# Performance work log

Hardware: AMD Instinct MI355X
Metric: run time of the kernel (lower is better)

The kernel has to match this reference:

```python
import jax, jax.numpy as jnp
import numpy as np

N_NODES = 100000


def setup_inputs() -> dict:
    key = jax.random.key(0)
    k1, k2, k3, k4, k5 = jax.random.split(key, 5)
    K, N, Z, F = 2, N_NODES, 128, 128
    E = 1600000
    x = jax.random.normal(k1, (K, N, Z), dtype=jnp.float32)
    adj_rows = jax.random.randint(k2, (E,), 0, N, dtype=jnp.int32)
    adj_cols = jax.random.randint(k3, (E,), 0, N, dtype=jnp.int32)
    adj_vals = jax.random.uniform(k4, (E,), dtype=jnp.float32)
    # xavier_uniform_ for [Z, F]
    limit = float(np.sqrt(6.0 / (Z + F)))
    weight = jax.random.uniform(k5, (Z, F), dtype=jnp.float32, minval=-limit, maxval=limit)
    return {"x": x, "adj_rows": adj_rows, "adj_cols": adj_cols,
            "adj_vals": adj_vals, "weight": weight}


def reference(x, adj_rows, adj_cols, adj_vals, weight):
    # dropout p=0.0 -> identity
    # support[k] = x[k] @ W  (shared weight across the K MIMO channels)
    support = jnp.einsum('knz,zf->knf', x, weight)  # [K, N, F]

    def spmm(sup):  # sparse adj (COO) @ dense [N, F]
        gathered = adj_vals[:, None] * sup[adj_cols]          # [E, F]
        return jax.ops.segment_sum(gathered, adj_rows, num_segments=N_NODES)

    # K is small and fixed; loop to avoid materializing [K, E, F] at once
    out = jnp.stack([spmm(support[k]) for k in range(support.shape[0])], axis=0)
    return jax.nn.relu(out)
```

## Files before the change

kernel.cpp:

```cpp
#include <hip/hip_runtime.h>

#define KCH 2
#define ZF 128
#define CHUNK 256
typedef unsigned short u16;

using bf16x8_t = __attribute__((ext_vector_type(8))) short;
using f32x4_t  = __attribute__((ext_vector_type(4))) float;
using f32x4n   = __attribute__((ext_vector_type(4))) float;

__device__ inline u16 f2bf(float f) {
  unsigned u = __float_as_uint(f);
  return (u16)((u + 0x7FFF + ((u >> 16) & 1)) >> 16);
}
__device__ inline float bf2f(u16 h) { return __uint_as_float((unsigned)h << 16); }

__global__ __launch_bounds__(256) void zero_and_wfrag(
    int* __restrict__ p, int n, int nbN,
    const float* __restrict__ W, u16* __restrict__ wf) {
  if ((int)blockIdx.x < nbN) {
    int i = blockIdx.x * 256 + threadIdx.x;
    if (i < n) p[i] = 0;
    return;
  }
  int t = (blockIdx.x - nbN) * 256 + threadIdx.x;
  if (t >= 16384) return;
  int k = t >> 7, f = t & 127;
  int ks = k >> 5, kk = k & 31;
  int lg = kk >> 3, j = kk & 7;
  int ft = f >> 4, c = f & 15;
  int l = lg * 16 + c;
  int e = ((ft * 4 + ks) * 64 + l) * 8 + j;
  float w = W[t];
  u16 hi = f2bf(w);
  u16 lo = f2bf(w - bf2f(hi));
  wf[e] = hi;
  wf[16384 + e] = lo;
}

__global__ __launch_bounds__(256) void hist_kernel(
    const int* __restrict__ rows, int* __restrict__ cnt, int E) {
  int i = blockIdx.x * 256 + threadIdx.x;
  if (i < E) atomicAdd(&cnt[rows[i]], 1);
}

__global__ __launch_bounds__(256) void chunk_reduce(
    const int* __restrict__ cnt, int* __restrict__ chunk, int N) {
  __shared__ int s[256];
  int tid = threadIdx.x;
  int i = blockIdx.x * 256 + tid;
  s[tid] = (i < N) ? cnt[i] : 0;
  __syncthreads();
#pragma unroll
  for (int o = 128; o > 0; o >>= 1) {
    if (tid < o) s[tid] += s[tid + o];
    __syncthreads();
  }
  if (tid == 0) chunk[blockIdx.x] = s[0];
}

__global__ __launch_bounds__(512) void chunk_scan(
    int* __restrict__ chunk, int nch, int* __restrict__ row_off, int N, int E) {
  __shared__ int s[512];
  int tid = threadIdx.x;
  int v = (tid < nch) ? chunk[tid] : 0;
  s[tid] = v;
  __syncthreads();
#pragma unroll
  for (int o = 1; o < 512; o <<= 1) {
    int t = (tid >= o) ? s[tid - o] : 0;
    __syncthreads();
    s[tid] += t;
    __syncthreads();
  }
  if (tid < nch) chunk[tid] = s[tid] - v;
  if (tid == 0) row_off[N] = E;
}

__global__ __launch_bounds__(256) void scan_within_chunk(
    const int* __restrict__ cnt, const int* __restrict__ chunk,
    int* __restrict__ row_off, int* __restrict__ cursor, int N) {
  __shared__ int s[256];
  int tid = threadIdx.x;
  int i = blockIdx.x * 256 + tid;
  int v = (i < N) ? cnt[i] : 0;
  s[tid] = v;
  __syncthreads();
#pragma unroll
  for (int o = 1; o < 256; o <<= 1) {
    int t = (tid >= o) ? s[tid - o] : 0;
    __syncthreads();
    s[tid] += t;
    __syncthreads();
  }
  if (i < N) {
    int start = chunk[blockIdx.x] + s[tid] - v;
    row_off[i] = start;
    cursor[i] = start;
  }
}

__global__ __launch_bounds__(256) void bucket_kernel(
    const int* __restrict__ rows, const int* __restrict__ cols,
    const float* __restrict__ vals, int* __restrict__ cursor,
    int2* __restrict__ pairs, int E) {
  int i = blockIdx.x * 256 + threadIdx.x;
  if (i >= E) return;
  int r = rows[i];
  int p = atomicAdd(&cursor[r], 1);
  int2 pr;
  pr.x = cols[i];
  pr.y = __float_as_int(vals[i]);
  pairs[p] = pr;
}

__global__ __launch_bounds__(256) void gemm_xw_bf16(
    const float* __restrict__ x, const u16* __restrict__ wf,
    u16* __restrict__ xi, int N) {
  __shared__ u16 lw[32768];
  int tid = threadIdx.x;
  {
    const uint4* src = (const uint4*)wf;
    uint4* dst = (uint4*)lw;
#pragma unroll
    for (int i = 0; i < 16; ++i) dst[tid + i * 256] = src[tid + i * 256];
  }
  __syncthreads();

  int l   = tid & 63;
  int col = l & 15;
  int rg  = l >> 4;
  int wgid = blockIdx.x * 4 + (tid >> 6);
  int nt = (KCH * N) >> 4;
  int nw = gridDim.x * 4;

  for (int t = wgid; t < nt; t += nw) {
    int row0 = t << 4;
    int kc = (row0 >= N) ? 1 : 0;
    int n0 = row0 - kc * N;

    const float* xb = x + (size_t)(kc * N + n0 + col) * ZF + rg * 8;
    bf16x8_t bhi[4], blo[4];
#pragma unroll
    for (int ks = 0; ks < 4; ++ks) {
      f32x4n u = __builtin_nontemporal_load((const f32x4n*)(xb + ks * 32));
      f32x4n v = __builtin_nontemporal_load(((const f32x4n*)(xb + ks * 32)) + 1);
      float tmp[8] = {u[0], u[1], u[2], u[3], v[0], v[1], v[2], v[3]};
#pragma unroll
      for (int j = 0; j < 8; ++j) {
        u16 hi = f2bf(tmp[j]);
        bhi[ks][j] = (short)hi;
        blo[ks][j] = (short)f2bf(tmp[j] - bf2f(hi));
      }
    }

    f32x4_t acc[8];
#pragma unroll
    for (int ft = 0; ft < 8; ++ft) acc[ft] = {0.f, 0.f, 0.f, 0.f};

#pragma unroll
    for (int ft = 0; ft < 8; ++ft) {
#pragma unroll
      for (int ks = 0; ks < 4; ++ks) {
        int eb = ((ft * 4 + ks) * 64 + l) * 8;
        const bf16x8_t ahi = *(const bf16x8_t*)(lw + eb);
        const bf16x8_t alo = *(const bf16x8_t*)(lw + 16384 + eb);
        acc[ft] = __builtin_amdgcn_mfma_f32_16x16x32_bf16(ahi, bhi[ks], acc[ft], 0, 0, 0);
        acc[ft] = __builtin_amdgcn_mfma_f32_16x16x32_bf16(alo, bhi[ks], acc[ft], 0, 0, 0);
        acc[ft] = __builtin_amdgcn_mfma_f32_16x16x32_bf16(ahi, blo[ks], acc[ft], 0, 0, 0);
      }
    }

    u16* dst = xi + (size_t)(n0 + col) * 256 + kc * 128;
#pragma unroll
    for (int ft = 0; ft < 8; ++ft) {
      ushort4 o;
      o.x = f2bf(acc[ft][0]);
      o.y = f2bf(acc[ft][1]);
      o.z = f2bf(acc[ft][2]);
      o.w = f2bf(acc[ft][3]);
      *(ushort4*)(dst + ft * 16 + rg * 4) = o;
    }
  }
}

__global__ __launch_bounds__(256) void spmm_csr_bf16(
    const u16* __restrict__ xi, const int* __restrict__ row_off,
    const int2* __restrict__ pairs, float* __restrict__ out, int N,
    int r0, int rcnt) {
  int rr = blockIdx.x * 4 + (threadIdx.x >> 6);
  if (rr >= rcnt) return;
  int r = r0 + rr;
  if (r >= N) return;
  int lane = threadIdx.x & 63;
  int beg = row_off[r];
  int end = row_off[r + 1];

  float4 acc = make_float4(0.f, 0.f, 0.f, 0.f);
  int j = beg;
  for (; j + 4 <= end; j += 4) {
    int2 p0 = pairs[j + 0];
    int2 p1 = pairs[j + 1];
    int2 p2 = pairs[j + 2];
    int2 p3 = pairs[j + 3];
    ushort4 a0 = ((const ushort4*)(xi + (size_t)p0.x * 256))[lane];
    ushort4 a1 = ((const ushort4*)(xi + (size_t)p1.x * 256))[lane];
    ushort4 a2 = ((const ushort4*)(xi + (size_t)p2.x * 256))[lane];
    ushort4 a3 = ((const ushort4*)(xi + (size_t)p3.x * 256))[lane];
    float v0 = __int_as_float(p0.y);
    float v1 = __int_as_float(p1.y);
    float v2 = __int_as_float(p2.y);
    float v3 = __int_as_float(p3.y);
    acc.x = fmaf(v0, bf2f(a0.x), acc.x);
    acc.y = fmaf(v0, bf2f(a0.y), acc.y);
    acc.z = fmaf(v0, bf2f(a0.z), acc.z);
    acc.w = fmaf(v0, bf2f(a0.w), acc.w);
    acc.x = fmaf(v1, bf2f(a1.x), acc.x);
    acc.y = fmaf(v1, bf2f(a1.y), acc.y);
    acc.z = fmaf(v1, bf2f(a1.z), acc.z);
    acc.w = fmaf(v1, bf2f(a1.w), acc.w);
    acc.x = fmaf(v2, bf2f(a2.x), acc.x);
    acc.y = fmaf(v2, bf2f(a2.y), acc.y);
    acc.z = fmaf(v2, bf2f(a2.z), acc.z);
    acc.w = fmaf(v2, bf2f(a2.w), acc.w);
    acc.x = fmaf(v3, bf2f(a3.x), acc.x);
    acc.y = fmaf(v3, bf2f(a3.y), acc.y);
    acc.z = fmaf(v3, bf2f(a3.z), acc.z);
    acc.w = fmaf(v3, bf2f(a3.w), acc.w);
  }
  for (; j < end; ++j) {
    int2 p = pairs[j];
    ushort4 a = ((const ushort4*)(xi + (size_t)p.x * 256))[lane];
    float v = __int_as_float(p.y);
    acc.x = fmaf(v, bf2f(a.x), acc.x);
    acc.y = fmaf(v, bf2f(a.y), acc.y);
    acc.z = fmaf(v, bf2f(a.z), acc.z);
    acc.w = fmaf(v, bf2f(a.w), acc.w);
  }
  f32x4n o;
  o[0] = fmaxf(acc.x, 0.f);
  o[1] = fmaxf(acc.y, 0.f);
  o[2] = fmaxf(acc.z, 0.f);
  o[3] = fmaxf(acc.w, 0.f);
  int k = lane >> 5;
  int g = lane & 31;
  __builtin_nontemporal_store(o, ((f32x4n*)(out + ((size_t)k * N + (size_t)r) * ZF)) + g);
}

__global__ __launch_bounds__(256) void spmm_csr(
    const float* __restrict__ x, const int* __restrict__ row_off,
    const int2* __restrict__ pairs, float* __restrict__ out, int N) {
  int r = blockIdx.x * 4 + (threadIdx.x >> 6);
  int lane = threadIdx.x & 63;
  if (r >= N) return;
  int k = lane >> 5;
  int g = lane & 31;
  int beg = row_off[r];
  int end = row_off[r + 1];
  const float* xb = x + (size_t)k * N * ZF;
  float4 acc = make_float4(0.f, 0.f, 0.f, 0.f);
  for (int j = beg; j < end; ++j) {
    int2 p = pairs[j];
    float4 a = ((const float4*)(xb + (size_t)p.x * ZF))[g];
    float v = __int_as_float(p.y);
    acc.x = fmaf(v, a.x, acc.x);
    acc.y = fmaf(v, a.y, acc.y);
    acc.z = fmaf(v, a.z, acc.z);
    acc.w = fmaf(v, a.w, acc.w);
  }
  ((float4*)(out + ((size_t)k * N + (size_t)r) * ZF))[g] = acc;
}

__device__ inline void atomic_add_f32(float* p, float v) {
#if defined(__HIP_DEVICE_COMPILE__) && defined(__AMDGCN__)
  unsafeAtomicAdd(p, v);
#else
  atomicAdd(p, v);
#endif
}

__global__ __launch_bounds__(256) void zero_kernel(float4* __restrict__ p, long long n4) {
  long long i = (long long)blockIdx.x * 256 + threadIdx.x;
  long long stride = (long long)gridDim.x * 256;
  for (; i < n4; i += stride) p[i] = make_float4(0.f, 0.f, 0.f, 0.f);
}

__global__ __launch_bounds__(256) void scatter_spmm_kernel(
    const float* __restrict__ x, const int* __restrict__ rows,
    const int* __restrict__ cols, const float* __restrict__ vals,
    float* __restrict__ tmp, int E, int N) {
  int t = blockIdx.x * 256 + threadIdx.x;
  int e = t >> 6;
  if (e >= E) return;
  int sub = t & 63;
  int k = sub >> 5;
  int g = sub & 31;
  int row = rows[e];
  int col = cols[e];
  float val = vals[e];
  const float4* src = (const float4*)(x + ((size_t)k * N + col) * ZF);
  float4 v = src[g];
  float* dst = tmp + ((size_t)k * N + row) * ZF + (size_t)g * 4;
  atomic_add_f32(dst + 0, val * v.x);
  atomic_add_f32(dst + 1, val * v.y);
  atomic_add_f32(dst + 2, val * v.z);
  atomic_add_f32(dst + 3, val * v.w);
}

__global__ __launch_bounds__(256) void gemm_relu_inplace(
    float* __restrict__ io, const float* __restrict__ W, long long Mtotal) {
  __shared__ float Ws[64 * ZF];
  __shared__ float Xs[32 * ZF];
  int tid = threadIdx.x;
  long long row0 = (long long)blockIdx.x * 32;

  const float4* src = (const float4*)(io + row0 * ZF);
  float4* Xs4 = (float4*)Xs;
#pragma unroll
  for (int i = 0; i < 4; ++i) {
    int idx = tid + i * 256;
    long long r = row0 + (idx >> 5);
    Xs4[idx] = (r < Mtotal) ? src[idx] : make_float4(0.f, 0.f, 0.f, 0.f);
  }

  int f0 = (tid & 31) * 4;
  int rg = tid >> 5;

  float acc[4][4];
#pragma unroll
  for (int j = 0; j < 4; ++j)
#pragma unroll
    for (int i = 0; i < 4; ++i) acc[j][i] = 0.f;

  const float4* W4 = (const float4*)W;
  float4* Ws4 = (float4*)Ws;

  for (int zh = 0; zh < 2; ++zh) {
    __syncthreads();
#pragma unroll
    for (int i = 0; i < 8; ++i) {
      int idx = tid + i * 256;
      Ws4[idx] = W4[(size_t)zh * 2048 + idx];
    }
    __syncthreads();

#pragma unroll 4
    for (int z = 0; z < 64; ++z) {
      float4 wv = *(const float4*)(Ws + z * ZF + f0);
#pragma unroll
      for (int j = 0; j < 4; ++j) {
        float xv = Xs[(rg + 8 * j) * ZF + (zh * 64 + z)];
        acc[j][0] = fmaf(xv, wv.x, acc[j][0]);
        acc[j][1] = fmaf(xv, wv.y, acc[j][1]);
        acc[j][2] = fmaf(xv, wv.z, acc[j][2]);
        acc[j][3] = fmaf(xv, wv.w, acc[j][3]);
      }
    }
  }

#pragma unroll
  for (int j = 0; j < 4; ++j) {
    long long r = row0 + rg + 8 * j;
    if (r < Mtotal) {
      float4 o;
      o.x = fmaxf(acc[j][0], 0.f);
      o.y = fmaxf(acc[j][1], 0.f);
      o.z = fmaxf(acc[j][2], 0.f);
      o.w = fmaxf(acc[j][3], 0.f);
      *(float4*)(io + r * ZF + f0) = o;
    }
  }
}

extern "C" void kernel_launch(void* const* d_in, const int* in_sizes, int n_in,
                              void* d_out, int out_size, void* d_ws, size_t ws_size,
                              hipStream_t stream) {
  const float* x    = (const float*)d_in[0];
  const int*   rows = (const int*)d_in[1];
  const int*   cols = (const int*)d_in[2];
  const float* vals = (const float*)d_in[3];
  const float* W    = (const float*)d_in[4];

  int E = in_sizes[1];
  int N = in_sizes[0] / (KCH * ZF);
  float* out = (float*)d_out;

  int nch = (N + CHUNK - 1) / CHUNK;

  size_t off = 0;
  auto carve = [&](size_t bytes) {
    size_t p = off;
    off += (bytes + 15) & ~(size_t)15;
    return (char*)d_ws + p;
  };
  int*  row_off = (int*)carve((size_t)(N + 1) * 4);
  int*  cursor  = (int*)carve((size_t)N * 4);
  int*  chunk   = (int*)carve((size_t)nch * 4);
  int2* pairs   = (int2*)carve((size_t)E * 8);
  size_t off_csr = off;
  u16*  wf      = (u16*)carve(65536);
  u16*  xi      = (u16*)carve((size_t)N * KCH * ZF * 2);

  bool csr_ok  = (off_csr <= ws_size) && (nch <= 512);
  bool bf16_ok = (off <= ws_size) && (nch <= 512) && ((N & 15) == 0);

  if (csr_ok) {
    int nb_N = (N + 255) / 256;
    int nb_E = (E + 255) / 256;

    int wblocks = bf16_ok ? 64 : 0;
    zero_and_wfrag<<<nb_N + wblocks, 256, 0, stream>>>(cursor, N, nb_N, W, wf);
    hist_kernel<<<nb_E, 256, 0, stream>>>(rows, cursor, E);
    chunk_reduce<<<nch, 256, 0, stream>>>(cursor, chunk, N);
    chunk_scan<<<1, 512, 0, stream>>>(chunk, nch, row_off, N, E);
    scan_within_chunk<<<nch, 256, 0, stream>>>(cursor, chunk, row_off, cursor, N);
    bucket_kernel<<<nb_E, 256, 0, stream>>>(rows, cols, vals, cursor, pairs, E);

    if (bf16_ok) {
      gemm_xw_bf16<<<512, 256, 0, stream>>>(x, wf, xi, N);
      int q = (N + 3) / 4;
      for (int i = 0; i < 4; ++i) {
        int r0 = i * q;
        int rcnt = (r0 + q <= N) ? q : (N - r0);
        if (rcnt <= 0) break;
        int blocks = (rcnt + 3) / 4;
        spmm_csr_bf16<<<blocks, 256, 0, stream>>>(xi, row_off, pairs, out, N, r0, rcnt);
      }
    } else {
      int sblocks = (N + 3) / 4;
      spmm_csr<<<sblocks, 256, 0, stream>>>(x, row_off, pairs, out, N);
      long long Mtotal = (long long)KCH * N;
      int mblocks = (int)((Mtotal + 31) / 32);
      gemm_relu_inplace<<<mblocks, 256, 0, stream>>>(out, W, Mtotal);
    }
  } else {
    long long n4 = (long long)out_size / 4;
    int zblocks = (int)((n4 + 255) / 256);
    zero_kernel<<<zblocks, 256, 0, stream>>>((float4*)out, n4);
    long long total_threads = (long long)E * 64;
    int sblocks = (int)((total_threads + 255) / 256);
    scatter_spmm_kernel<<<sblocks, 256, 0, stream>>>(x, rows, cols, vals, out, E, N);
    long long Mtotal = (long long)KCH * N;
    int mblocks = (int)((Mtotal + 31) / 32);
    gemm_relu_inplace<<<mblocks, 256, 0, stream>>>(out, W, Mtotal);
  }
}
```

Measured before the change: 552.0 us.

## Replace global-atomic CSR build with two-level binned counting sort

Builds the CSR structure with a coarse pass that bins edges into row buckets of 512 using block-local shared-memory histograms, then a per-bucket fine sort in shared memory. This replaces per-edge global atomics for the histogram and the scatter, which produced contention and random writes. Bin data is stored temporarily in the xi buffer before the GEMM overwrites it. The SpMM is also launched once over all rows instead of as four quarter launches.

After: 468.0 us. -15.2%, faster.

```diff
diff --git a/kernel.cpp b/kernel.cpp
--- a/kernel.cpp
+++ b/kernel.cpp
@@ -3,6 +3,7 @@
 #define KCH 2
 #define ZF 128
 #define CHUNK 256
+#define BSH 9
 typedef unsigned short u16;
 
 using bf16x8_t = __attribute__((ext_vector_type(8))) short;
@@ -36,6 +37,109 @@
   u16 lo = f2bf(w - bf2f(hi));
   wf[e] = hi;
   wf[16384 + e] = lo;
+}
+
+
+__global__ __launch_bounds__(256) void coarse_hist(
+    const int* __restrict__ rows, int* __restrict__ gcnt,
+    int E, int chunk, int NB) {
+  __shared__ int lc[256];
+  int t = threadIdx.x;
+  lc[t] = 0;
+  __syncthreads();
+  int b0 = blockIdx.x * chunk;
+  int b1 = min(E, b0 + chunk);
+  for (int i = b0 + t; i < b1; i += 256)
+    atomicAdd(&lc[rows[i] >> BSH], 1);
+  __syncthreads();
+  if (t < NB && lc[t]) atomicAdd(&gcnt[t], lc[t]);
+}
+
+__global__ __launch_bounds__(256) void bucket_scan(
+    int* __restrict__ cw, int NB, int E, int* __restrict__ row_off, int N) {
+  __shared__ int s[256];
+  int t = threadIdx.x;
+  int v = (t < NB) ? cw[t] : 0;
+  s[t] = v;
+  __syncthreads();
+#pragma unroll
+  for (int o = 1; o < 256; o <<= 1) {
+    int u = (t >= o) ? s[t - o] : 0;
+    __syncthreads();
+    s[t] += u;
+    __syncthreads();
+  }
+  int ex = s[t] - v;
+  if (t < NB) { cw[256 + t] = ex; cw[512 + t] = ex; }
+  if (t == 0) { cw[512 + NB] = E; row_off[N] = E; }
+}
+
+__global__ __launch_bounds__(256) void coarse_scatter(
+    const int* __restrict__ rows, const int* __restrict__ cols,
+    const float* __restrict__ vals, int* __restrict__ gcursor,
+    int2* __restrict__ binned_rc, float* __restrict__ binned_v,
+    int E, int chunk, int NB) {
+  __shared__ int lc[256];
+  __shared__ int lcur[256];
+  int t = threadIdx.x;
+  lc[t] = 0;
+  __syncthreads();
+  int b0 = blockIdx.x * chunk;
+  int b1 = min(E, b0 + chunk);
+  for (int i = b0 + t; i < b1; i += 256)
+    atomicAdd(&lc[rows[i] >> BSH], 1);
+  __syncthreads();
+  if (t < NB) lcur[t] = lc[t] ? atomicAdd(&gcursor[t], lc[t]) : 0;
+  __syncthreads();
+  for (int i = b0 + t; i < b1; i += 256) {
+    int r = rows[i];
+    int p = atomicAdd(&lcur[r >> BSH], 1);
+    binned_rc[p] = make_int2(r, cols[i]);
+    binned_v[p] = vals[i];
+  }
+}
+
+__global__ __launch_bounds__(256) void fine_sort(
+    const int2* __restrict__ binned_rc, const float* __restrict__ binned_v,
+    const int* __restrict__ bbase, int2* __restrict__ pairs,
+    int* __restrict__ row_off, int N) {
+  int b = blockIdx.x;
+  int beg = bbase[b];
+  int endb = bbase[b + 1];
+  int row0 = b << BSH;
+  int nr = min(1 << BSH, N - row0);
+  __shared__ int cnt[512];
+  __shared__ int s2[256];
+  __shared__ int cur[512];
+  int t = threadIdx.x;
+  cnt[t] = 0;
+  cnt[t + 256] = 0;
+  __syncthreads();
+  for (int i = beg + t; i < endb; i += 256)
+    atomicAdd(&cnt[binned_rc[i].x - row0], 1);
+  __syncthreads();
+  int c0 = cnt[2 * t], c1 = cnt[2 * t + 1];
+  s2[t] = c0 + c1;
+  __syncthreads();
+#pragma unroll
+  for (int o = 1; o < 256; o <<= 1) {
+    int u = (t >= o) ? s2[t - o] : 0;
+    __syncthreads();
+    s2[t] += u;
+    __syncthreads();
+  }
+  int exb = s2[t] - (c0 + c1);
+  cur[2 * t] = beg + exb;
+  cur[2 * t + 1] = beg + exb + c0;
+  if (2 * t < nr)     row_off[row0 + 2 * t]     = beg + exb;
+  if (2 * t + 1 < nr) row_off[row0 + 2 * t + 1] = beg + exb + c0;
+  __syncthreads();
+  for (int i = beg + t; i < endb; i += 256) {
+    int2 rc = binned_rc[i];
+    float v = binned_v[i];
+    int p = atomicAdd(&cur[rc.x - row0], 1);
+    pairs[p] = make_int2(rc.y, __float_as_int(v));
+  }
 }
 
 __global__ __launch_bounds__(256) void hist_kernel(
@@ -404,34 +508,50 @@
   bool csr_ok  = (off_csr <= ws_size) && (nch <= 512);
   bool bf16_ok = (off <= ws_size) && (nch <= 512) && ((N & 15) == 0);
 
+  int NB = (N + (1 << BSH) - 1) >> BSH;
+  bool binned_ok = bf16_ok && (NB <= 256) && (N >= 1024) &&
+                   ((size_t)E * 12 <= (size_t)N * KCH * ZF * 2);
+
   if (csr_ok) {
-    int nb_N = (N + 255) / 256;
     int nb_E = (E + 255) / 256;
 
-    int wblocks = bf16_ok ? 64 : 0;
-    zero_and_wfrag<<<nb_N + wblocks, 256, 0, stream>>>(cursor, N, nb_N, W, wf);
-    hist_kernel<<<nb_E, 256, 0, stream>>>(rows, cursor, E);
-    chunk_reduce<<<nch, 256, 0, stream>>>(cursor, chunk, N);
-    chunk_scan<<<1, 512, 0, stream>>>(chunk, nch, row_off, N, E);
-    scan_within_chunk<<<nch, 256, 0, stream>>>(cursor, chunk, row_off, cursor, N);
-    bucket_kernel<<<nb_E, 256, 0, stream>>>(rows, cols, vals, cursor, pairs, E);
-
-    if (bf16_ok) {
+    if (binned_ok) {
+      int2*  binned_rc = (int2*)xi;
+      float* binned_v  = (float*)((char*)xi + (size_t)E * 8);
+      int*   cw        = cursor;
+      int GA = 512;
+      int chunkE = (E + GA - 1) / GA;
+
+      zero_and_wfrag<<<1 + 64, 256, 0, stream>>>(cw, 256, 1, W, wf);
+      coarse_hist<<<GA, 256, 0, stream>>>(rows, cw, E, chunkE, NB);
+      bucket_scan<<<1, 256, 0, stream>>>(cw, NB, E, row_off, N);
+      coarse_scatter<<<GA, 256, 0, stream>>>(rows, cols, vals, cw + 256,
+                                             binned_rc, binned_v, E, chunkE, NB);
+      fine_sort<<<NB, 256, 0, stream>>>(binned_rc, binned_v, cw + 512,
+                                        pairs, row_off, N);
       gemm_xw_bf16<<<512, 256, 0, stream>>>(x, wf, xi, N);
-      int q = (N + 3) / 4;
-      for (int i = 0; i < 4; ++i) {
-        int r0 = i * q;
-        int rcnt = (r0 + q <= N) ? q : (N - r0);
-        if (rcnt <= 0) break;
-        int blocks = (rcnt + 3) / 4;
-        spmm_csr_bf16<<<blocks, 256, 0, stream>>>(xi, row_off, pairs, out, N, r0, rcnt);
+      int sblocks = (N + 3) / 4;
+      spmm_csr_bf16<<<sblocks, 256, 0, stream>>>(xi, row_off, pairs, out, N, 0, N);
+    } else {
+      int nb_N = (N + 255) / 256;
+      int wblocks = bf16_ok ? 64 : 0;
+      zero_and_wfrag<<<nb_N + wblocks, 256, 0, stream>>>(cursor, N, nb_N, W, wf);
+      hist_kernel<<<nb_E, 256, 0, stream>>>(rows, cursor, E);
+      chunk_reduce<<<nch, 256, 0, stream>>>(cursor, chunk, N);
+      chunk_scan<<<1, 512, 0, stream>>>(chunk, nch, row_off, N, E);
+      scan_within_chunk<<<nch, 256, 0, stream>>>(cursor, chunk, row_off, cursor, N);
+      bucket_kernel<<<nb_E, 256, 0, stream>>>(rows, cols, vals, cursor, pairs, E);
+
+      int sblocks = (N + 3) / 4;
+      if (bf16_ok) {
+        gemm_xw_bf16<<<512, 256, 0, stream>>>(x, wf, xi, N);
+        spmm_csr_bf16<<<sblocks, 256, 0, stream>>>(xi, row_off, pairs, out, N, 0, N);
+      } else {
+        spmm_csr<<<sblocks, 256, 0, stream>>>(x, row_off, pairs, out, N);
+        long long Mtotal = (long long)KCH * N;
+        int mblocks = (int)((Mtotal + 31) / 32);
+        gemm_relu_inplace<<<mblocks, 256, 0, stream>>>(out, W, Mtotal);
       }
-    } else {
-      int sblocks = (N + 3) / 4;
-      spmm_csr<<<sblocks, 256, 0, stream>>>(x, row_off, pairs, out, N);
-      long long Mtotal = (long long)KCH * N;
-      int mblocks = (int)((Mtotal + 31) / 32);
-      gemm_relu_inplace<<<mblocks, 256, 0, stream>>>(out, W, Mtotal);
     }
   } else {
     long long n4 = (long long)out_size / 4;
```
